# Kernel optimization log

Hardware: AMD Instinct MI355X
Metric: run time of the kernel (lower is better)

The kernel has to match this reference:

```python
import jax, jax.numpy as jnp
import numpy as np

HIDDEN = 1024
CUTOFFS = [20000, 80000, 200000]
PROJECT_FACTOR = 4
NUM_TAILS = len(CUTOFFS) - 1
CUTOFF_ENDS = [0] + CUTOFFS
BATCH, SEQ = 8, 1024


def _glorot(key, shape):
    fan_in, fan_out = shape
    limit = np.sqrt(6.0 / (fan_in + fan_out)).astype(np.float32)
    return jax.random.uniform(key, shape, jnp.float32, -limit, limit)


def setup_inputs() -> dict:
    key = jax.random.key(0)
    ks = jax.random.split(key, 7)
    return {
        "x": jax.random.randint(ks[0], (BATCH, SEQ), 0, CUTOFFS[-1], dtype=jnp.int64.dtype if jax.config.jax_enable_x64 else jnp.int32),
        "head_weight_proj": _glorot(ks[1], (HIDDEN, HIDDEN)),
        "head_weight": _glorot(ks[2], (HIDDEN, CUTOFFS[0] + NUM_TAILS)),
        "tail_weight_proj_0": _glorot(ks[3], (HIDDEN, HIDDEN // PROJECT_FACTOR)),
        "tail_weight_0": _glorot(ks[4], (HIDDEN // PROJECT_FACTOR, CUTOFFS[1] - CUTOFFS[0])),
        "tail_weight_proj_1": _glorot(ks[5], (HIDDEN, HIDDEN // PROJECT_FACTOR ** 2)),
        "tail_weight_1": _glorot(ks[6], (HIDDEN // PROJECT_FACTOR ** 2, CUTOFFS[2] - CUTOFFS[1])),
    }


def reference(x, head_weight_proj, head_weight, tail_weight_proj_0,
              tail_weight_0, tail_weight_proj_1, tail_weight_1) -> jnp.ndarray:
    # Faithful to AdaptiveEmbedding.compute_embeddings:
    #   tables[i] = weight.T (head truncated to cutoffs[0] rows), projs[i] = proj.T
    #   per-cluster: gather rows of table for in-range ids, matmul with proj,
    #   scatter back into y; here expressed densely with masks (same math,
    #   fixed shapes; out-of-cluster tokens contribute exactly zero).
    tables = [head_weight.T[:CUTOFFS[0]], tail_weight_0.T, tail_weight_1.T]
    projs = [head_weight_proj.T, tail_weight_proj_0.T, tail_weight_proj_1.T]
    y = jnp.zeros(x.shape + (HIDDEN,), dtype=jnp.float32)
    for i in range(len(CUTOFF_ENDS) - 1):
        l_idx, r_idx = CUTOFF_ENDS[i], CUTOFF_ENDS[i + 1]
        mask = (x >= l_idx) & (x < r_idx)                  # [B,S]
        idx = jnp.where(mask, x - l_idx, 0)                # in-range gather ids
        emb = tables[i][idx]                               # [B,S,d_i]
        proj = jnp.einsum('bsd,dh->bsh', emb, projs[i])    # [B,S,H]
        y = y + jnp.where(mask[..., None], proj, 0.0)
    emb_scale = jnp.asarray(HIDDEN ** 0.5, y.dtype)
    return y * emb_scale
```

## Files before the change

kernel.cpp:

```cpp
#include <hip/hip_runtime.h>
#include <hip/hip_bf16.h>

#define NTOK 8192
#define HID 1024
#define C0_END 20000
#define C1_END 80000

#define CAP0 1280
#define CAP1 3072
#define CAP2 6144
#define TS0 (CAP0/32)
#define TS1 (CAP1/32)
#define TS2 (CAP2/32)

#define OFF_CNT 0
#define OFF_LS  256
#define OFF_LI  (OFF_LS + NTOK*3*4)
#define OFF_W0  (OFF_LI + NTOK*3*4)
#define OFF_W1  (OFF_W0 + 1024*1024*2)
#define OFF_W2  (OFF_W1 + 1024*256*2)
#define OFF_A0  (OFF_W2 + 1024*64*2)
#define OFF_A1  (OFF_A0 + CAP0*1024*2)
#define OFF_A2  (OFF_A1 + CAP1*256*2)

typedef __attribute__((ext_vector_type(8))) short bf16x8;
typedef __attribute__((ext_vector_type(8))) unsigned short ushort8;
typedef __attribute__((ext_vector_type(4))) float f32x4;

__device__ __forceinline__ unsigned short f2bf(float f) {
    union { __hip_bfloat16 b; unsigned short u; } cv;
    cv.b = __float2bfloat16(f);
    return cv.u;
}


__global__ void k_zero(int* cnt) {
    if (threadIdx.x < 3) cnt[threadIdx.x] = 0;
}

__global__ void k_compact(const int* __restrict__ x, int* __restrict__ cnt,
                          int* __restrict__ ls, int* __restrict__ li) {
    int s = blockIdx.x * 256 + threadIdx.x;
    int lane = threadIdx.x & 63;
    int v = x[s];
    int c    = (v < C0_END) ? 0 : (v < C1_END ? 1 : 2);
    int base = (c == 0) ? 0 : (c == 1) ? C0_END : C1_END;
    int cap  = (c == 0) ? CAP0 : (c == 1) ? CAP1 : CAP2;
    unsigned long long m0 = __ballot(c == 0);
    unsigned long long m1 = __ballot(c == 1);
    unsigned long long m2 = __ballot(c == 2);
    unsigned long long mymask = (c == 0) ? m0 : (c == 1) ? m1 : m2;
    int leader = __builtin_ctzll(mymask);
    int wcount = __popcll(mymask);
    int rank   = __popcll(mymask & ((1ull << lane) - 1ull));
    int wbase = 0;
    if (lane == leader) wbase = atomicAdd(&cnt[c], wcount);
    wbase = __shfl(wbase, leader);
    int pos = wbase + rank;
    if (pos < cap) {
        ls[c * NTOK + pos] = s;
        li[c * NTOK + pos] = v - base;
    }
}

__global__ void k_gather(const float* __restrict__ t0, const float* __restrict__ t1,
                         const float* __restrict__ t2,
                         const float* __restrict__ hwp, const float* __restrict__ twp0,
                         const float* __restrict__ twp1,
                         const int* __restrict__ cnt, const int* __restrict__ li,
                         unsigned short* __restrict__ A0, unsigned short* __restrict__ A1,
                         unsigned short* __restrict__ A2,
                         unsigned short* __restrict__ W0, unsigned short* __restrict__ W1,
                         unsigned short* __restrict__ W2) {
    int gid = blockIdx.x * 256 + threadIdx.x, stride = gridDim.x * 256;
    for (int i = gid; i < (1024 * 1024) / 4; i += stride) {
        float4 v = ((const float4*)hwp)[i];
        ushort4 o = { f2bf(v.x), f2bf(v.y), f2bf(v.z), f2bf(v.w) };
        ((ushort4*)W0)[i] = o;
    }
    for (int i = gid; i < (1024 * 256) / 4; i += stride) {
        float4 v = ((const float4*)twp0)[i];
        ushort4 o = { f2bf(v.x), f2bf(v.y), f2bf(v.z), f2bf(v.w) };
        ((ushort4*)W1)[i] = o;
    }
    for (int i = gid; i < (1024 * 64) / 4; i += stride) {
        float4 v = ((const float4*)twp1)[i];
        ushort4 o = { f2bf(v.x), f2bf(v.y), f2bf(v.z), f2bf(v.w) };
        ((ushort4*)W2)[i] = o;
    }
    int n0 = min(cnt[0], CAP0), n1 = min(cnt[1], CAP1), n2 = min(cnt[2], CAP2);
    int r0 = ((n0 + 31) >> 5) << 5;
    int r1 = ((n1 + 31) >> 5) << 5;
    int r2 = ((n2 + 31) >> 5) << 5;
    int c0i = r0 << 7;
    int c1i = r1 << 5;
    int c2i = r2 << 3;
    int total = c0i + c1i + c2i;
    for (int e = gid; e < total; e += stride) {
        ushort8 v = {0, 0, 0, 0, 0, 0, 0, 0};
        unsigned short* dst;
        if (e < c0i) {
            int m = e >> 7, k8 = e & 127;
            if (m < n0) {
                const float* src = t0 + (size_t)k8 * 8 * 20002 + li[m];
#pragma unroll
                for (int j = 0; j < 8; j++) v[j] = f2bf(src[(size_t)j * 20002]);
            }
            int lane = (m & 15) + (k8 & 3) * 16;
            dst = A0 + (size_t)(((((m >> 5) * 32 + (k8 >> 2)) * 2) + ((m >> 4) & 1)) << 9)
                     + lane * 8;
        } else if (e < c0i + c1i) {
            int e1 = e - c0i;
            int m = e1 >> 5, k8 = e1 & 31;
            if (m < n1) {
                const float* src = t1 + (size_t)k8 * 8 * 60000 + li[NTOK + m];
#pragma unroll
                for (int j = 0; j < 8; j++) v[j] = f2bf(src[(size_t)j * 60000]);
            }
            int lane = (m & 15) + (k8 & 3) * 16;
            dst = A1 + (size_t)(((((m >> 5) * 8 + (k8 >> 2)) * 2) + ((m >> 4) & 1)) << 9)
                     + lane * 8;
        } else {
            int e2 = e - c0i - c1i;
            int m = e2 >> 3, k8 = e2 & 7;
            if (m < n2) {
                const float* src = t2 + (size_t)k8 * 8 * 120000 + li[2 * NTOK + m];
#pragma unroll
                for (int j = 0; j < 8; j++) v[j] = f2bf(src[(size_t)j * 120000]);
            }
            int lane = (m & 15) + (k8 & 3) * 16;
            dst = A2 + (size_t)(((((m >> 5) * 2 + (k8 >> 2)) * 2) + ((m >> 4) & 1)) << 9)
                     + lane * 8;
        }
        *(ushort8*)dst = v;
    }
}

template <int K>
__device__ __forceinline__ void gemm_body(int tile, int n, int lane, int wave, int by,
                                          const unsigned short* __restrict__ Ap,
                                          const unsigned short* __restrict__ Wb,
                                          const int* __restrict__ ls,
                                          float* __restrict__ out) {
    constexpr int KS = K / 32;
    int m0 = tile * 32;
    int lr = lane & 15, lg = lane >> 4;
    int hb = by * 256 + wave * 64;
    const unsigned short* abase = Ap + (size_t)tile * KS * 1024 + lane * 8;
    const unsigned short* bbase = Wb + (size_t)(hb + lr) * K + lg * 8;
    f32x4 acc[2][4] = {};
#pragma unroll 4
    for (int ks = 0; ks < KS; ks++) {
        bf16x8 a0 = *(const bf16x8*)(abase + ks * 1024);
        bf16x8 a1 = *(const bf16x8*)(abase + ks * 1024 + 512);
        bf16x8 b0 = *(const bf16x8*)(bbase + ks * 32);
        bf16x8 b1 = *(const bf16x8*)(bbase + ks * 32 + 16 * K);
        bf16x8 b2 = *(const bf16x8*)(bbase + ks * 32 + 32 * K);
        bf16x8 b3 = *(const bf16x8*)(bbase + ks * 32 + 48 * K);
        acc[0][0] = __builtin_amdgcn_mfma_f32_16x16x32_bf16(a0, b0, acc[0][0], 0, 0, 0);
        acc[0][1] = __builtin_amdgcn_mfma_f32_16x16x32_bf16(a0, b1, acc[0][1], 0, 0, 0);
        acc[0][2] = __builtin_amdgcn_mfma_f32_16x16x32_bf16(a0, b2, acc[0][2], 0, 0, 0);
        acc[0][3] = __builtin_amdgcn_mfma_f32_16x16x32_bf16(a0, b3, acc[0][3], 0, 0, 0);
        acc[1][0] = __builtin_amdgcn_mfma_f32_16x16x32_bf16(a1, b0, acc[1][0], 0, 0, 0);
        acc[1][1] = __builtin_amdgcn_mfma_f32_16x16x32_bf16(a1, b1, acc[1][1], 0, 0, 0);
        acc[1][2] = __builtin_amdgcn_mfma_f32_16x16x32_bf16(a1, b2, acc[1][2], 0, 0, 0);
        acc[1][3] = __builtin_amdgcn_mfma_f32_16x16x32_bf16(a1, b3, acc[1][3], 0, 0, 0);
    }
#pragma unroll
    for (int mf = 0; mf < 2; mf++)
#pragma unroll
        for (int r = 0; r < 4; r++) {
            int m = mf * 16 + lg * 4 + r;
            if (m0 + m < n) {
                int s = ls[m0 + m];
                float* orow = out + (size_t)s * HID + hb + lr;
                orow[0]  = 32.f * acc[mf][0][r];
                orow[16] = 32.f * acc[mf][1][r];
                orow[32] = 32.f * acc[mf][2][r];
                orow[48] = 32.f * acc[mf][3][r];
            }
        }
}

__global__ __launch_bounds__(256) void k_gemm(const int* __restrict__ cnt,
                                              const int* __restrict__ ls,
                                              const unsigned short* __restrict__ A0,
                                              const unsigned short* __restrict__ A1,
                                              const unsigned short* __restrict__ A2,
                                              const unsigned short* __restrict__ W0,
                                              const unsigned short* __restrict__ W1,
                                              const unsigned short* __restrict__ W2,
                                              float* __restrict__ out) {
    int bx = blockIdx.x;
    int lane = threadIdx.x & 63, wave = threadIdx.x >> 6;
    if (bx < TS0) {
        int n = min(cnt[0], CAP0); if (bx * 32 >= n) return;
        gemm_body<1024>(bx, n, lane, wave, blockIdx.y, A0, W0, ls, out);
    } else if (bx < TS0 + TS1) {
        int t = bx - TS0;
        int n = min(cnt[1], CAP1); if (t * 32 >= n) return;
        gemm_body<256>(t, n, lane, wave, blockIdx.y, A1, W1, ls + NTOK, out);
    } else {
        int t = bx - TS0 - TS1;
        int n = min(cnt[2], CAP2); if (t * 32 >= n) return;
        gemm_body<64>(t, n, lane, wave, blockIdx.y, A2, W2, ls + 2 * NTOK, out);
    }
}

extern "C" void kernel_launch(void* const* d_in, const int* in_sizes, int n_in,
                              void* d_out, int out_size, void* d_ws, size_t ws_size,
                              hipStream_t stream) {
    const int*   x    = (const int*)d_in[0];
    const float* hwp  = (const float*)d_in[1];
    const float* hw   = (const float*)d_in[2];
    const float* twp0 = (const float*)d_in[3];
    const float* tw0  = (const float*)d_in[4];
    const float* twp1 = (const float*)d_in[5];
    const float* tw1  = (const float*)d_in[6];

    char* ws = (char*)d_ws;
    int* cnt = (int*)(ws + OFF_CNT);
    int* ls  = (int*)(ws + OFF_LS);
    int* li  = (int*)(ws + OFF_LI);
    unsigned short* W0 = (unsigned short*)(ws + OFF_W0);
    unsigned short* W1 = (unsigned short*)(ws + OFF_W1);
    unsigned short* W2 = (unsigned short*)(ws + OFF_W2);
    unsigned short* A0 = (unsigned short*)(ws + OFF_A0);
    unsigned short* A1 = (unsigned short*)(ws + OFF_A1);
    unsigned short* A2 = (unsigned short*)(ws + OFF_A2);
    float* out = (float*)d_out;

    k_zero<<<1, 64, 0, stream>>>(cnt);
    k_compact<<<NTOK / 256, 256, 0, stream>>>(x, cnt, ls, li);
    k_gather<<<1024, 256, 0, stream>>>(hw, tw0, tw1, hwp, twp0, twp1,
                                       cnt, li, A0, A1, A2, W0, W1, W2);
    k_gemm<<<dim3(TS0 + TS1 + TS2, 4), 256, 0, stream>>>(
        cnt, ls, A0, A1, A2, W0, W1, W2, out);
}
```

Baseline: 79.26 us.

## Replace strided embedding gather with coalesced table streaming and reverse token lookup

The per-token strided column gather from the transposed embedding tables is replaced by a pass that streams all three tables row by row with coalesced float2 loads. During compaction, each token registers in a column-to-token map with linked lists for duplicate ids, and a bitmap marks which 4-column groups are referenced. The streaming pass skips unreferenced groups and scatters bf16 values into the MFMA fragment layout for every token that uses the column. This swaps random, poorly coalesced reads for a near-full sequential sweep of the tables, plus an init kernel and extra atomics. Padding rows of the A buffers are no longer zeroed.

```diff
diff --git a/kernel.cpp b/kernel.cpp
--- a/kernel.cpp
+++ b/kernel.cpp
@@ -5,6 +5,12 @@
 #define HID 1024
 #define C0_END 20000
 #define C1_END 80000
+#define V0 20000
+#define V1 60000
+#define V2 120000
+#define S0 20002
+#define S1 60000
+#define S2 120000
 
 #define CAP0 1280
 #define CAP1 3072
@@ -13,18 +19,27 @@
 #define TS1 (CAP1/32)
 #define TS2 (CAP2/32)
 
+#define WB0 0
+#define WB1 157
+#define WB2 626
+#define NBMPW 1564
+
 #define OFF_CNT 0
 #define OFF_LS  256
-#define OFF_LI  (OFF_LS + NTOK*3*4)
-#define OFF_W0  (OFF_LI + NTOK*3*4)
+#define OFF_W0  (OFF_LS + NTOK*3*4)
 #define OFF_W1  (OFF_W0 + 1024*1024*2)
 #define OFF_W2  (OFF_W1 + 1024*256*2)
 #define OFF_A0  (OFF_W2 + 1024*64*2)
 #define OFF_A1  (OFF_A0 + CAP0*1024*2)
 #define OFF_A2  (OFF_A1 + CAP1*256*2)
+#define OFF_CM0 (OFF_A2 + CAP2*64*2)
+#define OFF_CM1 (OFF_CM0 + 80128)
+#define OFF_CM2 (OFF_CM1 + 240128)
+#define OFF_NXT (OFF_CM2 + 480000)
+#define OFF_BMP (OFF_NXT + (CAP0+CAP1+CAP2)*4)
+#define NCMW    ((80128 + 240128 + 480000) / 4)
 
 typedef __attribute__((ext_vector_type(8))) short bf16x8;
-typedef __attribute__((ext_vector_type(8))) unsigned short ushort8;
 typedef __attribute__((ext_vector_type(4))) float f32x4;
 
 __device__ __forceinline__ unsigned short f2bf(float f) {
@@ -34,18 +49,26 @@
 }
 
 
-__global__ void k_zero(int* cnt) {
-    if (threadIdx.x < 3) cnt[threadIdx.x] = 0;
+__global__ void k_init(unsigned* __restrict__ cm, unsigned* __restrict__ bmp,
+                       int* __restrict__ cnt) {
+    int gid = blockIdx.x * 256 + threadIdx.x, stride = gridDim.x * 256;
+    for (int i = gid; i < NCMW; i += stride) cm[i] = 0xFFFFFFFFu;
+    for (int i = gid; i < NBMPW; i += stride) bmp[i] = 0u;
+    if (gid < 3) cnt[gid] = 0;
 }
 
 __global__ void k_compact(const int* __restrict__ x, int* __restrict__ cnt,
-                          int* __restrict__ ls, int* __restrict__ li) {
+                          int* __restrict__ ls,
+                          unsigned* __restrict__ cm0, unsigned* __restrict__ cm1,
+                          unsigned* __restrict__ cm2,
+                          int* __restrict__ nxt, unsigned* __restrict__ bmp) {
     int s = blockIdx.x * 256 + threadIdx.x;
     int lane = threadIdx.x & 63;
     int v = x[s];
     int c    = (v < C0_END) ? 0 : (v < C1_END ? 1 : 2);
     int base = (c == 0) ? 0 : (c == 1) ? C0_END : C1_END;
     int cap  = (c == 0) ? CAP0 : (c == 1) ? CAP1 : CAP2;
+    int idx  = v - base;
     unsigned long long m0 = __ballot(c == 0);
     unsigned long long m1 = __ballot(c == 1);
     unsigned long long m2 = __ballot(c == 2);
@@ -57,17 +80,64 @@
     if (lane == leader) wbase = atomicAdd(&cnt[c], wcount);
     wbase = __shfl(wbase, leader);
     int pos = wbase + rank;
+    int wb = (c == 0) ? WB0 : (c == 1) ? WB1 : WB2;
+    int q = idx >> 2;
+    atomicOr(&bmp[wb + (q >> 5)], 1u << (q & 31));
     if (pos < cap) {
         ls[c * NTOK + pos] = s;
-        li[c * NTOK + pos] = v - base;
-    }
-}
-
-__global__ void k_gather(const float* __restrict__ t0, const float* __restrict__ t1,
+        unsigned* cm = (c == 0) ? cm0 : (c == 1) ? cm1 : cm2;
+        int cb = (c == 0) ? 0 : (c == 1) ? CAP0 : CAP0 + CAP1;
+        unsigned old = atomicExch(&cm[idx], (unsigned)pos);
+        nxt[cb + pos] = (int)old;
+    }
+}
+
+template <int KS>
+__device__ __forceinline__ void frag_store(unsigned short* __restrict__ A,
+                                           unsigned m, int k, unsigned short v) {
+    size_t off = ((size_t)(((m >> 5) * KS + (k >> 5)) * 2 + ((m >> 4) & 1)) << 9)
+               + (size_t)(((m & 15) + ((k >> 3) & 3) * 16) * 8 + (k & 7));
+    A[off] = v;
+}
+
+template <int R, int V, int S, int CAPB, int WB, int KS>
+__device__ __forceinline__ void extract(int e, const float* __restrict__ t,
+                                        const unsigned* __restrict__ cm,
+                                        const unsigned* __restrict__ bmp,
+                                        const int* __restrict__ nxt,
+                                        unsigned short* __restrict__ A) {
+    constexpr int WQ = V / 4;
+    int k = e / WQ;
+    int q = e - k * WQ;
+    unsigned bw = bmp[WB + (q >> 5)];
+    if (!((bw >> (q & 31)) & 1u)) return;
+    int col = q * 4;
+    uint4 cmv = *(const uint4*)(cm + col);
+    const float* src = t + (size_t)k * S + col;
+    float2 lo = *(const float2*)(src);
+    float2 hi = *(const float2*)(src + 2);
+    float vals[4] = { lo.x, lo.y, hi.x, hi.y };
+    unsigned mm[4] = { cmv.x, cmv.y, cmv.z, cmv.w };
+#pragma unroll
+    for (int j = 0; j < 4; j++) {
+        unsigned m = mm[j];
+        if (m != 0xFFFFFFFFu) {
+            unsigned short v = f2bf(vals[j]);
+            do {
+                frag_store<KS>(A, m, k, v);
+                m = (unsigned)nxt[CAPB + m];
+            } while (m != 0xFFFFFFFFu);
+        }
+    }
+}
+
+__global__ void k_stream(const float* __restrict__ t0, const float* __restrict__ t1,
                          const float* __restrict__ t2,
                          const float* __restrict__ hwp, const float* __restrict__ twp0,
                          const float* __restrict__ twp1,
-                         const int* __restrict__ cnt, const int* __restrict__ li,
+                         const unsigned* __restrict__ cm0, const unsigned* __restrict__ cm1,
+                         const unsigned* __restrict__ cm2,
+                         const unsigned* __restrict__ bmp, const int* __restrict__ nxt,
                          unsigned short* __restrict__ A0, unsigned short* __restrict__ A1,
                          unsigned short* __restrict__ A2,
                          unsigned short* __restrict__ W0, unsigned short* __restrict__ W1,
@@ -88,51 +158,16 @@
         ushort4 o = { f2bf(v.x), f2bf(v.y), f2bf(v.z), f2bf(v.w) };
         ((ushort4*)W2)[i] = o;
     }
-    int n0 = min(cnt[0], CAP0), n1 = min(cnt[1], CAP1), n2 = min(cnt[2], CAP2);
-    int r0 = ((n0 + 31) >> 5) << 5;
-    int r1 = ((n1 + 31) >> 5) << 5;
-    int r2 = ((n2 + 31) >> 5) << 5;
-    int c0i = r0 << 7;
-    int c1i = r1 << 5;
-    int c2i = r2 << 3;
-    int total = c0i + c1i + c2i;
-    for (int e = gid; e < total; e += stride) {
-        ushort8 v = {0, 0, 0, 0, 0, 0, 0, 0};
-        unsigned short* dst;
-        if (e < c0i) {
-            int m = e >> 7, k8 = e & 127;
-            if (m < n0) {
-                const float* src = t0 + (size_t)k8 * 8 * 20002 + li[m];
-#pragma unroll
-                for (int j = 0; j < 8; j++) v[j] = f2bf(src[(size_t)j * 20002]);
-            }
-            int lane = (m & 15) + (k8 & 3) * 16;
-            dst = A0 + (size_t)(((((m >> 5) * 32 + (k8 >> 2)) * 2) + ((m >> 4) & 1)) << 9)
-                     + lane * 8;
-        } else if (e < c0i + c1i) {
-            int e1 = e - c0i;
-            int m = e1 >> 5, k8 = e1 & 31;
-            if (m < n1) {
-                const float* src = t1 + (size_t)k8 * 8 * 60000 + li[NTOK + m];
-#pragma unroll
-                for (int j = 0; j < 8; j++) v[j] = f2bf(src[(size_t)j * 60000]);
-            }
-            int lane = (m & 15) + (k8 & 3) * 16;
-            dst = A1 + (size_t)(((((m >> 5) * 8 + (k8 >> 2)) * 2) + ((m >> 4) & 1)) << 9)
-                     + lane * 8;
-        } else {
-            int e2 = e - c0i - c1i;
-            int m = e2 >> 3, k8 = e2 & 7;
-            if (m < n2) {
-                const float* src = t2 + (size_t)k8 * 8 * 120000 + li[2 * NTOK + m];
-#pragma unroll
-                for (int j = 0; j < 8; j++) v[j] = f2bf(src[(size_t)j * 120000]);
-            }
-            int lane = (m & 15) + (k8 & 3) * 16;
-            dst = A2 + (size_t)(((((m >> 5) * 2 + (k8 >> 2)) * 2) + ((m >> 4) & 1)) << 9)
-                     + lane * 8;
-        }
-        *(ushort8*)dst = v;
+    constexpr int T0N = 1024 * (V0 / 4);
+    constexpr int T1N = 256 * (V1 / 4);
+    constexpr int T2N = 64 * (V2 / 4);
+    for (int e = gid; e < T0N + T1N + T2N; e += stride) {
+        if (e < T0N)
+            extract<1024, V0, S0, 0, WB0, 32>(e, t0, cm0, bmp, nxt, A0);
+        else if (e < T0N + T1N)
+            extract<256, V1, S1, CAP0, WB1, 8>(e - T0N, t1, cm1, bmp, nxt, A1);
+        else
+            extract<64, V2, S2, CAP0 + CAP1, WB2, 2>(e - T0N - T1N, t2, cm2, bmp, nxt, A2);
     }
 }
 
@@ -221,19 +256,24 @@
     char* ws = (char*)d_ws;
     int* cnt = (int*)(ws + OFF_CNT);
     int* ls  = (int*)(ws + OFF_LS);
-    int* li  = (int*)(ws + OFF_LI);
     unsigned short* W0 = (unsigned short*)(ws + OFF_W0);
     unsigned short* W1 = (unsigned short*)(ws + OFF_W1);
     unsigned short* W2 = (unsigned short*)(ws + OFF_W2);
     unsigned short* A0 = (unsigned short*)(ws + OFF_A0);
     unsigned short* A1 = (unsigned short*)(ws + OFF_A1);
     unsigned short* A2 = (unsigned short*)(ws + OFF_A2);
+    unsigned* cm0 = (unsigned*)(ws + OFF_CM0);
+    unsigned* cm1 = (unsigned*)(ws + OFF_CM1);
+    unsigned* cm2 = (unsigned*)(ws + OFF_CM2);
+    int* nxt      = (int*)(ws + OFF_NXT);
+    unsigned* bmp = (unsigned*)(ws + OFF_BMP);
     float* out = (float*)d_out;
 
-    k_zero<<<1, 64, 0, stream>>>(cnt);
-    k_compact<<<NTOK / 256, 256, 0, stream>>>(x, cnt, ls, li);
-    k_gather<<<1024, 256, 0, stream>>>(hw, tw0, tw1, hwp, twp0, twp1,
-                                       cnt, li, A0, A1, A2, W0, W1, W2);
+    k_init<<<800, 256, 0, stream>>>(cm0, bmp, cnt);
+    k_compact<<<NTOK / 256, 256, 0, stream>>>(x, cnt, ls, cm0, cm1, cm2, nxt, bmp);
+    k_stream<<<8192, 256, 0, stream>>>(hw, tw0, tw1, hwp, twp0, twp1,
+                                       cm0, cm1, cm2, bmp, nxt,
+                                       A0, A1, A2, W0, W1, W2);
     k_gemm<<<dim3(TS0 + TS1 + TS2, 4), 256, 0, stream>>>(
         cnt, ls, A0, A1, A2, W0, W1, W2, out);
 }
```

After: 104.4 us. 1.32x slower.

## Bucket-sort token ids so gather reads neighboring table columns together

Applied to the files above, without the earlier changes.

Replaces the wave-ballot compaction with a counting sort: a histogram over 16-id buckets, a single-block prefix scan, and an atomic scatter, so each cluster's token list is ordered by embedding id. The gather loop is also reindexed to iterate over tokens fastest within each k8 slice. Together these make adjacent threads read nearby columns of the transposed fp32 tables, improving coalescing and cache-line reuse on strided gathers. The cost is two extra small kernel launches, 12.5K bucket atomics, and a serial one-block scan.

```diff
diff --git a/kernel.cpp b/kernel.cpp
--- a/kernel.cpp
+++ b/kernel.cpp
@@ -5,6 +5,9 @@
 #define HID 1024
 #define C0_END 20000
 #define C1_END 80000
+#define S0 20002
+#define S1 60000
+#define S2 120000
 
 #define CAP0 1280
 #define CAP1 3072
@@ -13,13 +16,17 @@
 #define TS1 (CAP1/32)
 #define TS2 (CAP2/32)
 
+#define NBUCK 12500
+
 #define OFF_CNT 0
-#define OFF_LS  256
+#define OFF_SST 16
+#define OFF_BB  32
+#define OFF_LS  50048
 #define OFF_LI  (OFF_LS + NTOK*3*4)
 #define OFF_W0  (OFF_LI + NTOK*3*4)
 #define OFF_W1  (OFF_W0 + 1024*1024*2)
-#define OFF_W2  (OFF_W1 + 1024*256*2)
-#define OFF_A0  (OFF_W2 + 1024*64*2)
+#define OFF_W2  (OFF_W1 + 256*1024*2)
+#define OFF_A0  (OFF_W2 + 64*1024*2)
 #define OFF_A1  (OFF_A0 + CAP0*1024*2)
 #define OFF_A2  (OFF_A1 + CAP1*256*2)
 
@@ -34,33 +41,86 @@
 }
 
 
-__global__ void k_zero(int* cnt) {
-    if (threadIdx.x < 3) cnt[threadIdx.x] = 0;
-}
-
-__global__ void k_compact(const int* __restrict__ x, int* __restrict__ cnt,
-                          int* __restrict__ ls, int* __restrict__ li) {
+__global__ void k_init(unsigned* __restrict__ bb, int* __restrict__ cnt) {
+    int gid = blockIdx.x * 256 + threadIdx.x, stride = gridDim.x * 256;
+    for (int i = gid; i < NBUCK; i += stride) bb[i] = 0u;
+    if (gid < 3) cnt[gid] = 0;
+}
+
+__global__ void k_count(const int* __restrict__ x, int* __restrict__ cnt,
+                        unsigned* __restrict__ bb) {
     int s = blockIdx.x * 256 + threadIdx.x;
     int lane = threadIdx.x & 63;
     int v = x[s];
-    int c    = (v < C0_END) ? 0 : (v < C1_END ? 1 : 2);
-    int base = (c == 0) ? 0 : (c == 1) ? C0_END : C1_END;
-    int cap  = (c == 0) ? CAP0 : (c == 1) ? CAP1 : CAP2;
+    atomicAdd(&bb[v >> 4], 1u);
+    int c = (v < C0_END) ? 0 : (v < C1_END ? 1 : 2);
     unsigned long long m0 = __ballot(c == 0);
     unsigned long long m1 = __ballot(c == 1);
     unsigned long long m2 = __ballot(c == 2);
     unsigned long long mymask = (c == 0) ? m0 : (c == 1) ? m1 : m2;
     int leader = __builtin_ctzll(mymask);
-    int wcount = __popcll(mymask);
-    int rank   = __popcll(mymask & ((1ull << lane) - 1ull));
-    int wbase = 0;
-    if (lane == leader) wbase = atomicAdd(&cnt[c], wcount);
-    wbase = __shfl(wbase, leader);
-    int pos = wbase + rank;
+    if (lane == leader) atomicAdd(&cnt[c], __popcll(mymask));
+}
+
+__global__ __launch_bounds__(1024) void k_scan(unsigned* __restrict__ bb,
+                                               unsigned* __restrict__ sstart) {
+    __shared__ unsigned psum[16];
+    int t = threadIdx.x, lane = t & 63, w = t >> 6;
+    int base = t * 13;
+    unsigned loc[13];
+    unsigned s = 0;
+#pragma unroll
+    for (int i = 0; i < 13; i++) {
+        int idx = base + i;
+        unsigned v = (idx < NBUCK) ? bb[idx] : 0u;
+        loc[i] = v; s += v;
+    }
+    unsigned inc = s;
+    for (int d = 1; d < 64; d <<= 1) {
+        unsigned o = __shfl_up(inc, d);
+        if (lane >= d) inc += o;
+    }
+    if (lane == 63) psum[w] = inc;
+    __syncthreads();
+    if (w == 0) {
+        unsigned ws = (lane < 16) ? psum[lane] : 0u;
+        for (int d = 1; d < 16; d <<= 1) {
+            unsigned o = __shfl_up(ws, d);
+            if (lane >= d) ws += o;
+        }
+        if (lane < 16) psum[lane] = ws;
+    }
+    __syncthreads();
+    unsigned excl = inc - s + ((w > 0) ? psum[w - 1] : 0u);
+#pragma unroll
+    for (int i = 0; i < 13; i++) {
+        int idx = base + i;
+        if (idx < NBUCK) bb[idx] = excl;
+        excl += loc[i];
+    }
+    __syncthreads();
+    if (t == 0) { sstart[0] = 0u; sstart[1] = bb[1250]; sstart[2] = bb[5000]; }
+}
+
+__global__ void k_scatter(const int* __restrict__ x, unsigned* __restrict__ bb,
+                          const unsigned* __restrict__ sstart,
+                          int* __restrict__ ls, int* __restrict__ li) {
+    int s = blockIdx.x * 256 + threadIdx.x;
+    int v = x[s];
+    int c    = (v < C0_END) ? 0 : (v < C1_END ? 1 : 2);
+    int base = (c == 0) ? 0 : (c == 1) ? C0_END : C1_END;
+    unsigned cap = (c == 0) ? CAP0 : (c == 1) ? CAP1 : CAP2;
+    unsigned pos = atomicAdd(&bb[v >> 4], 1u) - sstart[c];
     if (pos < cap) {
         ls[c * NTOK + pos] = s;
         li[c * NTOK + pos] = v - base;
     }
+}
+
+template <int KS>
+__device__ __forceinline__ size_t frag_off(int m, int k8) {
+    return ((size_t)(((m >> 5) * KS + (k8 >> 2)) * 2 + ((m >> 4) & 1)) << 9)
+         + (size_t)(((m & 15) + (k8 & 3) * 16) * 8);
 }
 
 __global__ void k_gather(const float* __restrict__ t0, const float* __restrict__ t1,
@@ -92,45 +152,39 @@
     int r0 = ((n0 + 31) >> 5) << 5;
     int r1 = ((n1 + 31) >> 5) << 5;
     int r2 = ((n2 + 31) >> 5) << 5;
-    int c0i = r0 << 7;
-    int c1i = r1 << 5;
-    int c2i = r2 << 3;
-    int total = c0i + c1i + c2i;
+    int i0 = r0 << 7;
+    int i1 = r1 << 5;
+    int i2 = r2 << 3;
+    int total = i0 + i1 + i2;
     for (int e = gid; e < total; e += stride) {
         ushort8 v = {0, 0, 0, 0, 0, 0, 0, 0};
         unsigned short* dst;
-        if (e < c0i) {
-            int m = e >> 7, k8 = e & 127;
+        if (e < i0) {
+            int k8 = e / r0, m = e - k8 * r0;
             if (m < n0) {
-                const float* src = t0 + (size_t)k8 * 8 * 20002 + li[m];
-#pragma unroll
-                for (int j = 0; j < 8; j++) v[j] = f2bf(src[(size_t)j * 20002]);
-            }
-            int lane = (m & 15) + (k8 & 3) * 16;
-            dst = A0 + (size_t)(((((m >> 5) * 32 + (k8 >> 2)) * 2) + ((m >> 4) & 1)) << 9)
-                     + lane * 8;
-        } else if (e < c0i + c1i) {
-            int e1 = e - c0i;
-            int m = e1 >> 5, k8 = e1 & 31;
+                const float* src = t0 + (size_t)k8 * 8 * S0 + li[m];
+#pragma unroll
+                for (int j = 0; j < 8; j++) v[j] = f2bf(src[(size_t)j * S0]);
+            }
+            dst = A0 + frag_off<32>(m, k8);
+        } else if (e < i0 + i1) {
+            int e1 = e - i0;
+            int k8 = e1 / r1, m = e1 - k8 * r1;
             if (m < n1) {
-                const float* src = t1 + (size_t)k8 * 8 * 60000 + li[NTOK + m];
-#pragma unroll
-                for (int j = 0; j < 8; j++) v[j] = f2bf(src[(size_t)j * 60000]);
-            }
-            int lane = (m & 15) + (k8 & 3) * 16;
-            dst = A1 + (size_t)(((((m >> 5) * 8 + (k8 >> 2)) * 2) + ((m >> 4) & 1)) << 9)
-                     + lane * 8;
+                const float* src = t1 + (size_t)k8 * 8 * S1 + li[NTOK + m];
+#pragma unroll
+                for (int j = 0; j < 8; j++) v[j] = f2bf(src[(size_t)j * S1]);
+            }
+            dst = A1 + frag_off<8>(m, k8);
         } else {
-            int e2 = e - c0i - c1i;
-            int m = e2 >> 3, k8 = e2 & 7;
+            int e2 = e - i0 - i1;
+            int k8 = e2 / r2, m = e2 - k8 * r2;
             if (m < n2) {
-                const float* src = t2 + (size_t)k8 * 8 * 120000 + li[2 * NTOK + m];
-#pragma unroll
-                for (int j = 0; j < 8; j++) v[j] = f2bf(src[(size_t)j * 120000]);
-            }
-            int lane = (m & 15) + (k8 & 3) * 16;
-            dst = A2 + (size_t)(((((m >> 5) * 2 + (k8 >> 2)) * 2) + ((m >> 4) & 1)) << 9)
-                     + lane * 8;
+                const float* src = t2 + (size_t)k8 * 8 * S2 + li[2 * NTOK + m];
+#pragma unroll
+                for (int j = 0; j < 8; j++) v[j] = f2bf(src[(size_t)j * S2]);
+            }
+            dst = A2 + frag_off<2>(m, k8);
         }
         *(ushort8*)dst = v;
     }
@@ -219,9 +273,11 @@
     const float* tw1  = (const float*)d_in[6];
 
     char* ws = (char*)d_ws;
-    int* cnt = (int*)(ws + OFF_CNT);
-    int* ls  = (int*)(ws + OFF_LS);
-    int* li  = (int*)(ws + OFF_LI);
+    int* cnt          = (int*)(ws + OFF_CNT);
+    unsigned* sstart  = (unsigned*)(ws + OFF_SST);
+    unsigned* bb      = (unsigned*)(ws + OFF_BB);
+    int* ls           = (int*)(ws + OFF_LS);
+    int* li           = (int*)(ws + OFF_LI);
     unsigned short* W0 = (unsigned short*)(ws + OFF_W0);
     unsigned short* W1 = (unsigned short*)(ws + OFF_W1);
     unsigned short* W2 = (unsigned short*)(ws + OFF_W2);
@@ -230,8 +286,10 @@
     unsigned short* A2 = (unsigned short*)(ws + OFF_A2);
     float* out = (float*)d_out;
 
-    k_zero<<<1, 64, 0, stream>>>(cnt);
-    k_compact<<<NTOK / 256, 256, 0, stream>>>(x, cnt, ls, li);
+    k_init<<<64, 256, 0, stream>>>(bb, cnt);
+    k_count<<<NTOK / 256, 256, 0, stream>>>(x, cnt, bb);
+    k_scan<<<1, 1024, 0, stream>>>(bb, sstart);
+    k_scatter<<<NTOK / 256, 256, 0, stream>>>(x, bb, sstart, ls, li);
     k_gather<<<1024, 256, 0, stream>>>(hw, tw0, tw1, hwp, twp0, twp1,
                                        cnt, li, A0, A1, A2, W0, W1, W2);
     k_gemm<<<dim3(TS0 + TS1 + TS2, 4), 256, 0, stream>>>(
```

Measured after the change: 77.34 us. 2.4% less time.
